# Performance work log

Hardware: AMD Instinct MI355X
Metric: run time of the kernel (lower is better)

## Reference

```python
import jax, jax.numpy as jnp
import numpy as np

B, IN, H = 4096, 1024, 1024


def setup_inputs() -> dict:
    key = jax.random.key(0)
    ks = jax.random.split(key, 16)
    s_in = 1.0 / np.sqrt(IN)
    s_h = 1.0 / np.sqrt(H)
    d = {
        "x_t": jax.random.normal(ks[0], (B, IN), jnp.float32),
        "h_prev": jax.random.normal(ks[1], (B, H), jnp.float32),
        "c_prev": jax.random.normal(ks[2], (B, H), jnp.float32),
    }
    # input->hidden weights (with bias), stored torch-style as (out, in)
    for i, name in enumerate(["ii", "if", "ig", "io"]):
        d[f"W_{name}"] = jax.random.uniform(ks[3 + i], (H, IN), jnp.float32, -s_in, s_in)
        d[f"b_{name}"] = jax.random.uniform(ks[7 + i], (H,), jnp.float32, -s_in, s_in)
    # hidden->hidden weights (no bias)
    for i, name in enumerate(["hi", "hf", "hg", "ho"]):
        d[f"W_{name}"] = jax.random.uniform(ks[11 + i], (H, H), jnp.float32, -s_h, s_h)
    return d


def reference(x_t, h_prev, c_prev,
              W_ii, b_ii, W_if, b_if, W_ig, b_ig, W_io, b_io,
              W_hi, W_hf, W_hg, W_ho):
    # Fuse the 8 small GEMMs into 2 concatenated GEMMs (same math).
    Wx = jnp.concatenate([W_ii, W_if, W_ig, W_io], axis=0)   # (4H, IN)
    Wh = jnp.concatenate([W_hi, W_hf, W_hg, W_ho], axis=0)   # (4H, H)
    b = jnp.concatenate([b_ii, b_if, b_ig, b_io], axis=0)    # (4H,)
    gates = x_t @ Wx.T + h_prev @ Wh.T + b                    # (B, 4H)
    zi, zf, zg, zo = jnp.split(gates, 4, axis=1)
    i_t = jax.nn.sigmoid(zi)
    f_t = jax.nn.sigmoid(zf)
    g_t = jnp.tanh(zg)
    o_t = jax.nn.sigmoid(zo)
    c_t = f_t * c_prev + i_t * g_t
    h_t = o_t * jnp.tanh(c_t)
    return (h_t, c_t, (i_t, f_t, g_t, o_t))
```

## Files before the change

### kernel.cpp

```cpp
#include <hip/hip_runtime.h>

#define B_DIM 4096
#define K_TOT 2048
#define H_DIM 1024

typedef short bf16x8 __attribute__((ext_vector_type(8)));
typedef float f32x4 __attribute__((ext_vector_type(4)));
typedef unsigned short u16x8 __attribute__((ext_vector_type(8)));

typedef __attribute__((address_space(1))) const unsigned gas_u32;
typedef __attribute__((address_space(3))) unsigned las_u32;

static __device__ __forceinline__ unsigned short f2bf(float f) {
  union { float f; unsigned u; } v; v.f = f;
  unsigned r = v.u + 0x7FFF + ((v.u >> 16) & 1);
  return (unsigned short)(r >> 16);
}

__global__ void pack_all(const float* __restrict__ x, const float* __restrict__ hp,
                         const float* __restrict__ W0, const float* __restrict__ W1,
                         const float* __restrict__ W2, const float* __restrict__ W3,
                         const float* __restrict__ W4, const float* __restrict__ W5,
                         const float* __restrict__ W6, const float* __restrict__ W7,
                         u16x8* __restrict__ A, u16x8* __restrict__ Wc) {
  const int t = blockIdx.x * blockDim.x + threadIdx.x;
  const int NA = (B_DIM * K_TOT) >> 3;
  const float* src;
  u16x8* dst;
  if (t < NA) {
    int idx = t << 3;
    int b = idx >> 11;
    int k = idx & 2047;
    src = (k < 1024) ? (x + b * 1024 + k) : (hp + b * 1024 + (k - 1024));
    dst = A + t;
  } else {
    int u_ = t - NA;
    int idx = u_ << 3;
    int R = idx >> 11;
    int k = idx & 2047;
    int uu = R & 255;
    int gate = (uu >> 4) & 3;
    int ngg = uu >> 6;
    int cc = uu & 15;
    int j = (R >> 8) * 64 + ngg * 16 + cc;
    int s = (k < 1024) ? gate : gate + 4;
    const float* base =
        (s == 0) ? W0 : (s == 1) ? W1 : (s == 2) ? W2 : (s == 3) ? W3 :
        (s == 4) ? W4 : (s == 5) ? W5 : (s == 6) ? W6 : W7;
    src = base + j * 1024 + (k & 1023);
    dst = Wc + u_;
  }
  float4 lo = *(const float4*)src;
  float4 hi = *(const float4*)(src + 4);
  u16x8 v;
  v[0] = f2bf(lo.x); v[1] = f2bf(lo.y); v[2] = f2bf(lo.z); v[3] = f2bf(lo.w);
  v[4] = f2bf(hi.x); v[5] = f2bf(hi.y); v[6] = f2bf(hi.z); v[7] = f2bf(hi.w);
  *dst = v;
}

static __device__ __forceinline__ float sigm(float x) {
  return 1.0f / (1.0f + __expf(-x));
}
static __device__ __forceinline__ float tanh_fast(float x) {
  x = fminf(fmaxf(x, -15.f), 15.f);
  float t = __expf(-2.0f * x);
  return (1.0f - t) / (1.0f + t);
}

__global__ __launch_bounds__(512, 2) void gemm_lstm(
    const unsigned short* __restrict__ A,
    const unsigned short* __restrict__ W,
    const float* __restrict__ cp,
    const float* __restrict__ bii, const float* __restrict__ bif,
    const float* __restrict__ big, const float* __restrict__ bio,
    float* __restrict__ out) {
  extern __shared__ char lds[];
  const int tid = threadIdx.x;
  const int w = tid >> 6;
  const int lane = tid & 63;
  const int wm = w >> 2;
  const int ng = w & 3;
  const int bx = blockIdx.x;
  const int by = blockIdx.y;

  f32x4 acc[8][4];
#pragma unroll
  for (int i = 0; i < 8; ++i)
#pragma unroll
    for (int n = 0; n < 4; ++n)
      acc[i][n] = (f32x4){0.f, 0.f, 0.f, 0.f};

  const int v0 = tid, v1 = tid + 512;
  const int r0 = v0 >> 2, g0 = (v0 & 3) ^ ((r0 >> 1) & 3);
  const int r1 = v1 >> 2, g1 = (v1 & 3) ^ ((r1 >> 1) & 3);
  const unsigned short* srcA0 = A + (long)(by * 256 + r0) * K_TOT + g0 * 8;
  const unsigned short* srcA1 = A + (long)(by * 256 + r1) * K_TOT + g1 * 8;
  const unsigned short* srcB0 = W + (long)(bx * 256 + r0) * K_TOT + g0 * 8;
  const unsigned short* srcB1 = W + (long)(bx * 256 + r1) * K_TOT + g1 * 8;
  const int d0 = v0 << 4, d1 = v1 << 4;

  const int fr = lane & 15;
  const int gg = lane >> 4;
  const int aoff = fr * 64 + ((gg ^ ((fr >> 1) & 3)) << 4);
  const int wmoff = wm << 13;
  const int ngoff = ng << 12;

  bf16x8 bfr[4];

#define STAGE(H)                                                               \
  {                                                                            \
    const int H_ = (H);                                                        \
    const int koff_ = (H_ >> 1) * 32;                                          \
    char* dst_ = lds + (((H_ >> 2) & 1) << 16) + ((H_ & 1) << 15) +            \
                 (((H_ >> 1) & 1) << 14);                                      \
    if (H_ & 1) {                                                              \
      __builtin_amdgcn_global_load_lds((gas_u32*)(srcB0 + koff_),              \
                                       (las_u32*)(dst_ + d0), 16, 0, 0);       \
      __builtin_amdgcn_global_load_lds((gas_u32*)(srcB1 + koff_),              \
                                       (las_u32*)(dst_ + d1), 16, 0, 0);       \
    } else {                                                                   \
      __builtin_amdgcn_global_load_lds((gas_u32*)(srcA0 + koff_),              \
                                       (las_u32*)(dst_ + d0), 16, 0, 0);       \
      __builtin_amdgcn_global_load_lds((gas_u32*)(srcA1 + koff_),              \
                                       (las_u32*)(dst_ + d1), 16, 0, 0);       \
    }                                                                          \
  }

#define G8 asm volatile("s_waitcnt vmcnt(8)" ::: "memory")
#define G4 asm volatile("s_waitcnt vmcnt(4)" ::: "memory")
#define G0 asm volatile("s_waitcnt vmcnt(0)" ::: "memory")
#define GN ((void)0)

#define DO_PHASE(P, KT, GUARD, DOSTAGE)                                        \
  {                                                                            \
    const char* lA_ = ldsbuf + ((P) >> 1) * 16384;                             \
    const char* lB_ = ldsbuf + 32768 + ((P) >> 1) * 16384;                     \
    bf16x8 af_[4];                                                             \
    _Pragma("unroll")                                                          \
    for (int i_ = 0; i_ < 4; ++i_)                                             \
      af_[i_] = *(const bf16x8*)(lA_ + wmoff + (((P) & 1) * 4 + i_) * 1024 + aoff); \
    if (((P) & 1) == 0) {                                                      \
      _Pragma("unroll")                                                        \
      for (int n_ = 0; n_ < 4; ++n_)                                           \
        bfr[n_] = *(const bf16x8*)(lB_ + ngoff + n_ * 1024 + aoff);            \
    }                                                                          \
    if (DOSTAGE) STAGE((KT) * 4 + (P) + 6);                                    \
    GUARD;                                                                     \
    __builtin_amdgcn_s_barrier();                                              \
    asm volatile("s_waitcnt lgkmcnt(0)" ::: "memory");                         \
    __builtin_amdgcn_sched_barrier(0);                                         \
    __builtin_amdgcn_s_setprio(1);                                             \
    _Pragma("unroll")                                                          \
    for (int i_ = 0; i_ < 4; ++i_) {                                           \
      _Pragma("unroll")                                                        \
      for (int n_ = 0; n_ < 4; ++n_)                                           \
        acc[((P) & 1) * 4 + i_][n_] = __builtin_amdgcn_mfma_f32_16x16x32_bf16( \
            af_[i_], bfr[n_], acc[((P) & 1) * 4 + i_][n_], 0, 0, 0);           \
    }                                                                          \
    __builtin_amdgcn_s_setprio(0);                                             \
    __builtin_amdgcn_s_barrier();                                              \
  }

  STAGE(0); STAGE(1); STAGE(2); STAGE(3); STAGE(4); STAGE(5);
  asm volatile("s_waitcnt vmcnt(8)" ::: "memory");
  __builtin_amdgcn_s_barrier();

  for (int kt = 0; kt < 30; ++kt) {
    const char* ldsbuf = lds + ((kt & 1) << 16);
    DO_PHASE(0, kt, GN, 1);
    DO_PHASE(1, kt, G8, 1);
    DO_PHASE(2, kt, GN, 1);
    DO_PHASE(3, kt, G8, 1);
  }
  {
    const char* ldsbuf = lds;
    DO_PHASE(0, 30, GN, 1);
    DO_PHASE(1, 30, G8, 1);
    DO_PHASE(2, 30, GN, 0);
    DO_PHASE(3, 30, G4, 0);
  }
  {
    const char* ldsbuf = lds + 65536;
    DO_PHASE(0, 31, GN, 0);
    DO_PHASE(1, 31, G0, 0);
    DO_PHASE(2, 31, GN, 0);
    DO_PHASE(3, 31, GN, 0);
  }
#undef DO_PHASE
#undef STAGE

  const int ccol = lane & 15;
  const int crow = (lane >> 4) << 2;
  const int j = (bx << 6) + (ng << 4) + ccol;
  const float bi = bii[j];
  const float bff = bif[j];
  const float bg = big[j];
  const float bo = bio[j];
  const long BH = (long)B_DIM * H_DIM;
  const int row0 = (by << 8) + (wm << 7) + crow;
#pragma unroll
  for (int mi = 0; mi < 8; ++mi) {
#pragma unroll
    for (int reg = 0; reg < 4; ++reg) {
      const int row = row0 + mi * 16 + reg;
      const long p = (long)row * H_DIM + j;
      const float cvp = cp[p];
      const float iv = sigm(acc[mi][0][reg] + bi);
      const float fv = sigm(acc[mi][1][reg] + bff);
      const float gv = tanh_fast(acc[mi][2][reg] + bg);
      const float ov = sigm(acc[mi][3][reg] + bo);
      const float cv = fv * cvp + iv * gv;
      const float hv = ov * tanh_fast(cv);
      out[p]          = hv;
      out[BH + p]     = cv;
      out[2 * BH + p] = iv;
      out[3 * BH + p] = fv;
      out[4 * BH + p] = gv;
      out[5 * BH + p] = ov;
    }
  }
}

extern "C" void kernel_launch(void* const* d_in, const int* in_sizes, int n_in,
                              void* d_out, int out_size, void* d_ws, size_t ws_size,
                              hipStream_t stream) {
  const float* x    = (const float*)d_in[0];
  const float* h    = (const float*)d_in[1];
  const float* c    = (const float*)d_in[2];
  const float* W_ii = (const float*)d_in[3];
  const float* b_ii = (const float*)d_in[4];
  const float* W_if = (const float*)d_in[5];
  const float* b_if = (const float*)d_in[6];
  const float* W_ig = (const float*)d_in[7];
  const float* b_ig = (const float*)d_in[8];
  const float* W_io = (const float*)d_in[9];
  const float* b_io = (const float*)d_in[10];
  const float* W_hi = (const float*)d_in[11];
  const float* W_hf = (const float*)d_in[12];
  const float* W_hg = (const float*)d_in[13];
  const float* W_ho = (const float*)d_in[14];

  unsigned short* Abf = (unsigned short*)d_ws;
  unsigned short* Wbf = (unsigned short*)((char*)d_ws + (size_t)16 * 1024 * 1024);

  static bool s_attr = false;
  if (!s_attr) {
    hipFuncSetAttribute((const void*)gemm_lstm,
                        hipFuncAttributeMaxDynamicSharedMemorySize, 131072);
    s_attr = true;
  }

  pack_all<<<8192, 256, 0, stream>>>(x, h, W_ii, W_if, W_ig, W_io,
                                     W_hi, W_hf, W_hg, W_ho,
                                     (u16x8*)Abf, (u16x8*)Wbf);
  dim3 grid(H_DIM / 64, B_DIM / 256);
  gemm_lstm<<<grid, 512, 131072, stream>>>(Abf, Wbf, c, b_ii, b_if, b_ig, b_io,
                                           (float*)d_out);
}
```

Measured before the change: 259.6 us.

## Pre-tile packed operands so GEMM stage loads are fully contiguous

The pack kernel now writes A and W in a tile-major order that already matches the swizzled LDS layout of each 256-row by 32-wide K slice. The GEMM's stage loads then become linear 16-byte copies from a contiguous 16KB chunk per stage, instead of strided row accesses with swizzle math. This aims to improve global load coalescing and cut address arithmetic in the main loop. In exchange the pack kernel reads its fp32 sources in a more scattered order.

New measurement: 256.7 us. About the same (-1.1%).

```diff
diff --git a/kernel.cpp b/kernel.cpp
--- a/kernel.cpp
+++ b/kernel.cpp
@@ -24,38 +24,44 @@
                          const float* __restrict__ W6, const float* __restrict__ W7,
                          u16x8* __restrict__ A, u16x8* __restrict__ Wc) {
   const int t = blockIdx.x * blockDim.x + threadIdx.x;
-  const int NA = (B_DIM * K_TOT) >> 3;
+  const int NA = 1 << 20;
   const float* src;
   u16x8* dst;
   if (t < NA) {
-    int idx = t << 3;
-    int b = idx >> 11;
-    int k = idx & 2047;
-    src = (k < 1024) ? (x + b * 1024 + k) : (hp + b * 1024 + (k - 1024));
+    int by = t >> 16;
+    int rem = t & 65535;
+    int half = rem >> 10;
+    int v = rem & 1023;
+    int r = v >> 2;
+    int g = (v & 3) ^ ((r >> 1) & 3);
+    int k = half * 32 + g * 8;
+    int row = by * 256 + r;
+    src = (k < 1024) ? (x + row * 1024 + k) : (hp + row * 1024 + (k - 1024));
     dst = A + t;
   } else {
-    int u_ = t - NA;
-    int idx = u_ << 3;
-    int R = idx >> 11;
-    int k = idx & 2047;
-    int uu = R & 255;
-    int gate = (uu >> 4) & 3;
-    int ngg = uu >> 6;
-    int cc = uu & 15;
-    int j = (R >> 8) * 64 + ngg * 16 + cc;
+    int u = t - NA;
+    int bx = u >> 16;
+    int rem = u & 65535;
+    int half = rem >> 10;
+    int v = rem & 1023;
+    int r = v >> 2;
+    int g = (v & 3) ^ ((r >> 1) & 3);
+    int k = half * 32 + g * 8;
+    int gate = (r >> 4) & 3;
+    int j = bx * 64 + (r >> 6) * 16 + (r & 15);
     int s = (k < 1024) ? gate : gate + 4;
     const float* base =
         (s == 0) ? W0 : (s == 1) ? W1 : (s == 2) ? W2 : (s == 3) ? W3 :
         (s == 4) ? W4 : (s == 5) ? W5 : (s == 6) ? W6 : W7;
     src = base + j * 1024 + (k & 1023);
-    dst = Wc + u_;
+    dst = Wc + u;
   }
   float4 lo = *(const float4*)src;
   float4 hi = *(const float4*)(src + 4);
-  u16x8 v;
-  v[0] = f2bf(lo.x); v[1] = f2bf(lo.y); v[2] = f2bf(lo.z); v[3] = f2bf(lo.w);
-  v[4] = f2bf(hi.x); v[5] = f2bf(hi.y); v[6] = f2bf(hi.z); v[7] = f2bf(hi.w);
-  *dst = v;
+  u16x8 v8;
+  v8[0] = f2bf(lo.x); v8[1] = f2bf(lo.y); v8[2] = f2bf(lo.z); v8[3] = f2bf(lo.w);
+  v8[4] = f2bf(hi.x); v8[5] = f2bf(hi.y); v8[6] = f2bf(hi.z); v8[7] = f2bf(hi.w);
+  *dst = v8;
 }
 
 static __device__ __forceinline__ float sigm(float x) {
@@ -90,14 +96,8 @@
     for (int n = 0; n < 4; ++n)
       acc[i][n] = (f32x4){0.f, 0.f, 0.f, 0.f};
 
-  const int v0 = tid, v1 = tid + 512;
-  const int r0 = v0 >> 2, g0 = (v0 & 3) ^ ((r0 >> 1) & 3);
-  const int r1 = v1 >> 2, g1 = (v1 & 3) ^ ((r1 >> 1) & 3);
-  const unsigned short* srcA0 = A + (long)(by * 256 + r0) * K_TOT + g0 * 8;
-  const unsigned short* srcA1 = A + (long)(by * 256 + r1) * K_TOT + g1 * 8;
-  const unsigned short* srcB0 = W + (long)(bx * 256 + r0) * K_TOT + g0 * 8;
-  const unsigned short* srcB1 = W + (long)(bx * 256 + r1) * K_TOT + g1 * 8;
-  const int d0 = v0 << 4, d1 = v1 << 4;
+  const unsigned short* Ap = A + (size_t)by * 524288;
+  const unsigned short* Wp = W + (size_t)bx * 524288;
 
   const int fr = lane & 15;
   const int gg = lane >> 4;
@@ -107,23 +107,17 @@
 
   bf16x8 bfr[4];
 
-#define STAGE(H)                                                               \
-  {                                                                            \
-    const int H_ = (H);                                                        \
-    const int koff_ = (H_ >> 1) * 32;                                          \
-    char* dst_ = lds + (((H_ >> 2) & 1) << 16) + ((H_ & 1) << 15) +            \
-                 (((H_ >> 1) & 1) << 14);                                      \
-    if (H_ & 1) {                                                              \
-      __builtin_amdgcn_global_load_lds((gas_u32*)(srcB0 + koff_),              \
-                                       (las_u32*)(dst_ + d0), 16, 0, 0);       \
-      __builtin_amdgcn_global_load_lds((gas_u32*)(srcB1 + koff_),              \
-                                       (las_u32*)(dst_ + d1), 16, 0, 0);       \
-    } else {                                                                   \
-      __builtin_amdgcn_global_load_lds((gas_u32*)(srcA0 + koff_),              \
-                                       (las_u32*)(dst_ + d0), 16, 0, 0);       \
-      __builtin_amdgcn_global_load_lds((gas_u32*)(srcA1 + koff_),              \
-                                       (las_u32*)(dst_ + d1), 16, 0, 0);       \
-    }                                                                          \
+#define STAGE(H)                                                                      \
+  {                                                                                   \
+    const int H_ = (H);                                                               \
+    char* dst_ = lds + (((H_ >> 2) & 1) << 16) + ((H_ & 1) << 15) +                   \
+                 (((H_ >> 1) & 1) << 14);                                             \
+    const unsigned short* s_ =                                                        \
+        ((H_ & 1) ? Wp : Ap) + ((((H_ >> 2) << 1) | ((H_ >> 1) & 1)) * 8192);         \
+    __builtin_amdgcn_global_load_lds((gas_u32*)(s_ + (size_t)tid * 8),                \
+                                     (las_u32*)(dst_ + tid * 16), 16, 0, 0);          \
+    __builtin_amdgcn_global_load_lds((gas_u32*)(s_ + (size_t)(tid + 512) * 8),        \
+                                     (las_u32*)(dst_ + (tid + 512) * 16), 16, 0, 0);  \
   }
 
 #define G8 asm volatile("s_waitcnt vmcnt(8)" ::: "memory")
```
